# Kernel optimization log

Measured on AMD Instinct MI355X. Metric: run time of the kernel, lower is better.

The kernel has to match this reference:

```python
import jax, jax.numpy as jnp
import numpy as np

# irreps_in = irreps_out = 64x0e + 32x1o
MUL0, MUL1 = 64, 32          # multiplicities of 0e scalars and 1o vectors
DIM_IN = MUL0 + MUL1 * 3     # 160
N_NODES = 50000
IU0, IV0 = np.triu_indices(MUL0, k=1)   # 2016 scalar u<v pairs
IU1, IV1 = np.triu_indices(MUL1, k=1)   # 496 vector u<v pairs
# e3nn path normalization (component / element):
#   i_out=0 (0e): num_elements sum = 2016 + 64 + 496 + 32 = 2608, dim(0e)=1
#   i_out=1 (1o): num_elements = 32*64 = 2048, dim(1o)=3
C0 = float(np.sqrt(1.0 / 2608.0))
C1 = float(np.sqrt(3.0 / 2048.0))
INV_SQRT3 = float(1.0 / np.sqrt(3.0))   # w3j(1,0,1) and w3j(1,1,0) CG factor


def setup_inputs() -> dict:
    key = jax.random.key(0)
    ks = jax.random.split(key, 7)
    node_feats = jax.random.normal(ks[0], (N_NODES, DIM_IN), jnp.float32)
    node_messages = jax.random.normal(ks[1], (N_NODES, DIM_IN), jnp.float32)
    W1 = jax.random.normal(ks[2], (len(IU0), MUL0), jnp.float32)  # (0e,0e)->0e u<vw
    W2 = jax.random.normal(ks[3], (MUL0, MUL0), jnp.float32)      # (0e,0e)->0e uuw
    W3 = jax.random.normal(ks[4], (MUL1, MUL0, MUL1), jnp.float32)  # (1o,0e)->1o uvw
    W4 = jax.random.normal(ks[5], (len(IU1), MUL0), jnp.float32)  # (1o,1o)->0e u<vw
    W5 = jax.random.normal(ks[6], (MUL1, MUL0), jnp.float32)      # (1o,1o)->0e uuw
    return {"node_feats": node_feats, "node_messages": node_messages,
            "W1": W1, "W2": W2, "W3": W3, "W4": W4, "W5": W5}


def _tensor_square(x, W1, W2, W3, W4, W5):
    x0 = x[:, :MUL0]                        # [N, 64] scalars (0e)
    x1 = x[:, MUL0:].reshape(-1, MUL1, 3)   # [N, 32, 3] vectors (1o)
    # (0e x 0e) -> 0e
    pair0 = x0[:, IU0] * x0[:, IV0]         # [N, 2016]
    sq0 = x0 * x0                           # [N, 64]
    # (1o x 1o) -> 0e via dot products (w3j(1,1,0) = delta/sqrt3)
    d = jnp.einsum('nui,nvi->nuv', x1, x1)  # [N, 32, 32]
    pair1 = d[:, IU1, IV1] * INV_SQRT3      # [N, 496]
    diag1 = jnp.einsum('nui,nui->nu', x1, x1) * INV_SQRT3  # [N, 32]
    out0 = C0 * (pair0 @ W1 + sq0 @ W2 + pair1 @ W4 + diag1 @ W5)  # [N, 64]
    # (1o x 0e) -> 1o fully connected uvw (w3j(1,0,1) = eye/sqrt3)
    out1 = (C1 * INV_SQRT3) * jnp.einsum('nui,nv,uvw->nwi', x1, x0, W3)  # [N,32,3]
    return jnp.concatenate([out0, out1.reshape(-1, MUL1 * 3)], axis=1)


def reference(node_feats, node_messages, W1, W2, W3, W4, W5):
    x = node_feats + node_messages
    return _tensor_square(x, W1, W2, W3, W4, W5)
```

## Files before the change

kernel.cpp:

```cpp
#include <hip/hip_runtime.h>

typedef unsigned short u16;
typedef unsigned int u32;

#define N_NODES 50000
#define NB      64

#define BG_OFF  0
#define BT_OFF  262144
#define BH_OFF  327680

#define ASTR   72
#define AHSTR  40
#define XTSTR  68

typedef __attribute__((ext_vector_type(8))) short short8;
typedef __attribute__((ext_vector_type(4))) float f32x4;
union U4S8 { uint4 u; short8 s; };

__device__ __forceinline__ u16 f2bf(float f) {
    u32 u = __float_as_uint(f);
    return (u16)((u + 0x7fffu + ((u >> 16) & 1u)) >> 16);
}
__device__ __forceinline__ f32x4 bf4(uint2 q) {
    f32x4 r;
    r[0] = __uint_as_float(q.x << 16);
    r[1] = __uint_as_float(q.x & 0xffff0000u);
    r[2] = __uint_as_float(q.y << 16);
    r[3] = __uint_as_float(q.y & 0xffff0000u);
    return r;
}

__global__ __launch_bounds__(256)
void pack_kernel(const float* __restrict__ W1, const float* __restrict__ W2,
                 const float* __restrict__ W3, const float* __restrict__ W4,
                 const float* __restrict__ W5, u16* __restrict__ ws) {
    const float INV_SQRT3 = 0.57735026918962576f;
    int T = blockIdx.x * 256 + threadIdx.x;
    int slot0 = T * 8;
    float vals[8];
    if (slot0 < BT_OFF) {
        int ntile = slot0 >> 10, rem = slot0 & 1023;
        int ks = rem >> 9, q = (rem & 511) >> 3;
        int vbase = ks * 32 + (q >> 4) * 8;
        int j = ntile * 16 + (q & 15);
        int u = j >> 6, w = j & 63;
        #pragma unroll
        for (int jj = 0; jj < 8; ++jj) {
            int v = vbase + jj;
            if (v == u) vals[jj] = W2[u * 64 + w];
            else {
                int a = min(u, v), b = max(u, v);
                int p = a * (127 - a) / 2 + (b - a - 1);
                vals[jj] = 0.5f * W1[p * 64 + w];
            }
        }
    } else if (slot0 < BH_OFF) {
        int s = slot0 - BT_OFF;
        int ntile = s >> 10, rem = s & 1023;
        int ks = rem >> 9, q = (rem & 511) >> 3;
        int vbase = ks * 32 + (q >> 4) * 8;
        int j = ntile * 16 + (q & 15);
        int u = j >> 5, w = j & 31;
        #pragma unroll
        for (int jj = 0; jj < 8; ++jj)
            vals[jj] = W3[(u * 64 + (vbase + jj)) * 32 + w];
    } else {
        int s = slot0 - BH_OFF;
        int ntile = s >> 9, q = (s & 511) >> 3;
        int vbase = (q >> 4) * 8;
        int j = ntile * 16 + (q & 15);
        int u = j >> 6, w = j & 63;
        #pragma unroll
        for (int jj = 0; jj < 8; ++jj) {
            int v = vbase + jj;
            if (v == u) vals[jj] = W5[u * 64 + w] * INV_SQRT3;
            else {
                int a = min(u, v), b = max(u, v);
                int p = a * (63 - a) / 2 + (b - a - 1);
                vals[jj] = (0.5f * INV_SQRT3) * W4[p * 64 + w];
            }
        }
    }
    uint4 o;
    o.x = ((u32)f2bf(vals[1]) << 16) | f2bf(vals[0]);
    o.y = ((u32)f2bf(vals[3]) << 16) | f2bf(vals[2]);
    o.z = ((u32)f2bf(vals[5]) << 16) | f2bf(vals[4]);
    o.w = ((u32)f2bf(vals[7]) << 16) | f2bf(vals[6]);
    *(uint4*)(ws + slot0) = o;
}

__global__ __launch_bounds__(256, 3)
void node_block_kernel(const float* __restrict__ feats, const float* __restrict__ msgs,
                       const u16* __restrict__ ws, float* __restrict__ out) {
    __shared__ u16 A_S[64 * ASTR];
    __shared__ u16 A_H[192 * AHSTR];
    __shared__ u16 x0T[64 * XTSTR];
    __shared__ u16 x1T[96 * XTSTR];

    const int tid = threadIdx.x;
    const int node0 = blockIdx.x * NB;

    for (int k = 0; k < 5; ++k) {
        int chunk = tid + k * 256;
        int idx = chunk * 8;
        int n = (u32)idx / 160u;
        int d = idx - n * 160;
        int g = node0 * 160 + idx;
        float v[8];
        if (g + 8 <= N_NODES * 160) {
            float4 fa0 = *(const float4*)(feats + g);
            float4 fa1 = *(const float4*)(feats + g + 4);
            float4 fb0 = *(const float4*)(msgs + g);
            float4 fb1 = *(const float4*)(msgs + g + 4);
            v[0]=fa0.x+fb0.x; v[1]=fa0.y+fb0.y; v[2]=fa0.z+fb0.z; v[3]=fa0.w+fb0.w;
            v[4]=fa1.x+fb1.x; v[5]=fa1.y+fb1.y; v[6]=fa1.z+fb1.z; v[7]=fa1.w+fb1.w;
        } else {
            #pragma unroll
            for (int j = 0; j < 8; ++j) v[j] = 0.f;
        }
        u16 bv[8];
        #pragma unroll
        for (int j = 0; j < 8; ++j) bv[j] = f2bf(v[j]);
        if (d < 64) {
            uint4 pk;
            pk.x = ((u32)bv[1] << 16) | bv[0];
            pk.y = ((u32)bv[3] << 16) | bv[2];
            pk.z = ((u32)bv[5] << 16) | bv[4];
            pk.w = ((u32)bv[7] << 16) | bv[6];
            *(uint4*)&A_S[n * ASTR + d] = pk;
            #pragma unroll
            for (int j = 0; j < 8; ++j) x0T[(d + j) * XTSTR + n] = bv[j];
        } else {
            #pragma unroll
            for (int j = 0; j < 8; ++j) {
                int dd = d + j - 64;
                int u = (u32)dd / 3u, i = dd - u * 3;
                A_H[(i * 64 + n) * AHSTR + u] = bv[j];
                x1T[(u * 3 + i) * XTSTR + n] = bv[j];
            }
        }
    }
    __syncthreads();

    const int wave = tid >> 6, lane = tid & 63, quad = lane >> 4, l15 = lane & 15;
    const int wq = wave;
    const f32x4 z4 = {0.f, 0.f, 0.f, 0.f};
    const int ph64 = (blockIdx.x * 5) & 63;
    const int ph32 = (blockIdx.x * 5) & 31;

    f32x4 o0[4];
    #pragma unroll
    for (int mt = 0; mt < 4; ++mt) o0[mt] = z4;

    {
        short8 aS[4][2];
        #pragma unroll
        for (int mt = 0; mt < 4; ++mt)
            #pragma unroll
            for (int ks = 0; ks < 2; ++ks) {
                U4S8 t; t.u = *(const uint4*)&A_S[(mt * 16 + l15) * ASTR + ks * 32 + quad * 8];
                aS[mt][ks] = t.s;
            }
        const u16* bp = ws + BG_OFF + (u32)wq * 1024 + lane * 8;
        U4S8 b0[2], b1[2];
        b0[0].u = *(const uint4*)(bp + ph64 * 4096);
        b1[0].u = *(const uint4*)(bp + ph64 * 4096 + 512);
        {
            int p1 = ((ph64 + 1) & 63) * 4096;
            b0[1].u = *(const uint4*)(bp + p1);
            b1[1].u = *(const uint4*)(bp + p1 + 512);
        }
        #pragma unroll 2
        for (int t = 0; t < 64; ++t) {
            const int c = t & 1;
            const int u = (ph64 + t) & 63;
            short8 B0 = b0[c].s, B1 = b1[c].s;
            if (t < 62) {
                int pp = ((ph64 + t + 2) & 63) * 4096;
                b0[c].u = *(const uint4*)(bp + pp);
                b1[c].u = *(const uint4*)(bp + pp + 512);
            }
            f32x4 acc[4];
            #pragma unroll
            for (int mt = 0; mt < 4; ++mt) acc[mt] = z4;
            #pragma unroll
            for (int mt = 0; mt < 4; ++mt)
                acc[mt] = __builtin_amdgcn_mfma_f32_16x16x32_bf16(aS[mt][0], B0, acc[mt], 0, 0, 0);
            #pragma unroll
            for (int mt = 0; mt < 4; ++mt)
                acc[mt] = __builtin_amdgcn_mfma_f32_16x16x32_bf16(aS[mt][1], B1, acc[mt], 0, 0, 0);
            #pragma unroll
            for (int mt = 0; mt < 4; ++mt) {
                f32x4 xq = bf4(*(const uint2*)&x0T[u * XTSTR + mt * 16 + quad * 4]);
                o0[mt] += xq * acc[mt];
            }
        }
    }

    {
        short8 aH[12];
        #pragma unroll
        for (int m = 0; m < 12; ++m) {
            U4S8 t; t.u = *(const uint4*)&A_H[(m * 16 + l15) * AHSTR + quad * 8];
            aH[m] = t.s;
        }
        const u16* bp = ws + BH_OFF + (u32)wq * 512 + lane * 8;
        U4S8 bb[2];
        bb[0].u = *(const uint4*)(bp + ph32 * 2048);
        bb[1].u = *(const uint4*)(bp + ((ph32 + 1) & 31) * 2048);
        #pragma unroll 2
        for (int t = 0; t < 32; ++t) {
            const int c = t & 1;
            const int u = (ph32 + t) & 31;
            short8 B = bb[c].s;
            if (t < 30) bb[c].u = *(const uint4*)(bp + ((ph32 + t + 2) & 31) * 2048);
            #pragma unroll
            for (int i = 0; i < 3; ++i) {
                f32x4 acc[4];
                #pragma unroll
                for (int m = 0; m < 4; ++m) acc[m] = z4;
                #pragma unroll
                for (int m = 0; m < 4; ++m)
                    acc[m] = __builtin_amdgcn_mfma_f32_16x16x32_bf16(aH[i * 4 + m], B, acc[m], 0, 0, 0);
                #pragma unroll
                for (int m = 0; m < 4; ++m) {
                    f32x4 xq = bf4(*(const uint2*)&x1T[(u * 3 + i) * XTSTR + m * 16 + quad * 4]);
                    o0[m] += xq * acc[m];
                }
            }
        }
    }

    {
        const float C0v = 0.019581512f;
        #pragma unroll
        for (int mt = 0; mt < 4; ++mt)
            #pragma unroll
            for (int rr = 0; rr < 4; ++rr) {
                int node = node0 + mt * 16 + quad * 4 + rr;
                if (node < N_NODES)
                    out[node * 160 + wq * 16 + l15] = C0v * o0[mt][rr];
            }
    }

    {
        const int mh = wave >> 1, wh = wave & 1;
        short8 aT[2][2];
        #pragma unroll
        for (int m = 0; m < 2; ++m)
            #pragma unroll
            for (int ks = 0; ks < 2; ++ks) {
                U4S8 t; t.u = *(const uint4*)&A_S[((mh * 2 + m) * 16 + l15) * ASTR + ks * 32 + quad * 8];
                aT[m][ks] = t.s;
            }
        f32x4 o1[3][2];
        #pragma unroll
        for (int i = 0; i < 3; ++i)
            #pragma unroll
            for (int m = 0; m < 2; ++m) o1[i][m] = z4;

        const u16* bp = ws + BT_OFF + (u32)wh * 1024 + lane * 8;
        U4S8 b0[2], b1[2];
        b0[0].u = *(const uint4*)(bp + ph32 * 2048);
        b1[0].u = *(const uint4*)(bp + ph32 * 2048 + 512);
        {
            int p1 = ((ph32 + 1) & 31) * 2048;
            b0[1].u = *(const uint4*)(bp + p1);
            b1[1].u = *(const uint4*)(bp + p1 + 512);
        }
        #pragma unroll 2
        for (int t = 0; t < 32; ++t) {
            const int c = t & 1;
            const int u = (ph32 + t) & 31;
            short8 B0 = b0[c].s, B1 = b1[c].s;
            if (t < 30) {
                int pp = ((ph32 + t + 2) & 31) * 2048;
                b0[c].u = *(const uint4*)(bp + pp);
                b1[c].u = *(const uint4*)(bp + pp + 512);
            }
            f32x4 acc[2];
            #pragma unroll
            for (int m = 0; m < 2; ++m) acc[m] = z4;
            #pragma unroll
            for (int m = 0; m < 2; ++m)
                acc[m] = __builtin_amdgcn_mfma_f32_16x16x32_bf16(aT[m][0], B0, acc[m], 0, 0, 0);
            #pragma unroll
            for (int m = 0; m < 2; ++m)
                acc[m] = __builtin_amdgcn_mfma_f32_16x16x32_bf16(aT[m][1], B1, acc[m], 0, 0, 0);
            #pragma unroll
            for (int i = 0; i < 3; ++i)
                #pragma unroll
                for (int m = 0; m < 2; ++m) {
                    f32x4 xq = bf4(*(const uint2*)&x1T[(u * 3 + i) * XTSTR + (mh * 2 + m) * 16 + quad * 4]);
                    o1[i][m] += xq * acc[m];
                }
        }
        const float S1 = 0.022097087f;
        #pragma unroll
        for (int i = 0; i < 3; ++i)
            #pragma unroll
            for (int m = 0; m < 2; ++m)
                #pragma unroll
                for (int rr = 0; rr < 4; ++rr) {
                    int node = node0 + (mh * 2 + m) * 16 + quad * 4 + rr;
                    if (node < N_NODES)
                        out[node * 160 + 64 + (wh * 16 + l15) * 3 + i] = S1 * o1[i][m][rr];
                }
    }
}

extern "C" void kernel_launch(void* const* d_in, const int* in_sizes, int n_in,
                              void* d_out, int out_size, void* d_ws, size_t ws_size,
                              hipStream_t stream) {
    const float* feats = (const float*)d_in[0];
    const float* msgs  = (const float*)d_in[1];
    const float* W1    = (const float*)d_in[2];
    const float* W2    = (const float*)d_in[3];
    const float* W3    = (const float*)d_in[4];
    const float* W4    = (const float*)d_in[5];
    const float* W5    = (const float*)d_in[6];
    float* out = (float*)d_out;
    u16* ws = (u16*)d_ws;

    hipLaunchKernelGGL(pack_kernel, dim3(192), dim3(256), 0, stream,
                       W1, W2, W3, W4, W5, ws);
    hipLaunchKernelGGL(node_block_kernel, dim3((N_NODES + NB - 1) / NB), dim3(256), 0, stream,
                       feats, msgs, ws, out);
}
```

Measured before the change: 195.8 us.

## Regroup scalar/vector LDS tiles by node quads and process two u per iteration

Replaces the transposed x0T/x1T and A_H shared-memory layouts with node-quad grouped x0G/x1G arrays, so each lane fetches the x-values for two consecutive u with one 16-byte LDS read. The loops now handle two u per iteration with a deeper B-fragment prefetch. The A_H buffer is removed and its fragments are gathered element-wise from x1G. The smaller LDS footprint allows launch bounds to rise to 4 blocks per CU. The costs are more register pressure, slower scalar gathers for the aH fragments, and a different phase-stagger pattern across blocks.

```diff
diff --git a/kernel.cpp b/kernel.cpp
--- a/kernel.cpp
+++ b/kernel.cpp
@@ -11,8 +11,8 @@
 #define BH_OFF  327680
 
 #define ASTR   72
-#define AHSTR  40
-#define XTSTR  68
+#define X0STR  66
+#define X1STR  98
 
 typedef __attribute__((ext_vector_type(8))) short short8;
 typedef __attribute__((ext_vector_type(4))) float f32x4;
@@ -90,13 +90,12 @@
     *(uint4*)(ws + slot0) = o;
 }
 
-__global__ __launch_bounds__(256, 3)
+__global__ __launch_bounds__(256, 4)
 void node_block_kernel(const float* __restrict__ feats, const float* __restrict__ msgs,
                        const u16* __restrict__ ws, float* __restrict__ out) {
     __shared__ u16 A_S[64 * ASTR];
-    __shared__ u16 A_H[192 * AHSTR];
-    __shared__ u16 x0T[64 * XTSTR];
-    __shared__ u16 x1T[96 * XTSTR];
+    __shared__ u16 x0G[16 * X0STR * 4];
+    __shared__ u16 x1G[16 * X1STR * 4];
 
     const int tid = threadIdx.x;
     const int node0 = blockIdx.x * NB;
@@ -129,15 +128,15 @@
             pk.z = ((u32)bv[5] << 16) | bv[4];
             pk.w = ((u32)bv[7] << 16) | bv[6];
             *(uint4*)&A_S[n * ASTR + d] = pk;
-            #pragma unroll
-            for (int j = 0; j < 8; ++j) x0T[(d + j) * XTSTR + n] = bv[j];
+            int b0 = ((n >> 2) * X0STR + d) * 4 + (n & 3);
+            #pragma unroll
+            for (int j = 0; j < 8; ++j) x0G[b0 + j * 4] = bv[j];
         } else {
             #pragma unroll
             for (int j = 0; j < 8; ++j) {
                 int dd = d + j - 64;
                 int u = (u32)dd / 3u, i = dd - u * 3;
-                A_H[(i * 64 + n) * AHSTR + u] = bv[j];
-                x1T[(u * 3 + i) * XTSTR + n] = bv[j];
+                x1G[((n >> 2) * X1STR + i * 32 + u) * 4 + (n & 3)] = bv[j];
             }
         }
     }
@@ -146,8 +145,8 @@
     const int wave = tid >> 6, lane = tid & 63, quad = lane >> 4, l15 = lane & 15;
     const int wq = wave;
     const f32x4 z4 = {0.f, 0.f, 0.f, 0.f};
-    const int ph64 = (blockIdx.x * 5) & 63;
-    const int ph32 = (blockIdx.x * 5) & 31;
+    const int ph64 = (blockIdx.x * 10) & 62;
+    const int ph32 = ph64 & 30;
 
     f32x4 o0[4];
     #pragma unroll
@@ -163,37 +162,52 @@
                 aS[mt][ks] = t.s;
             }
         const u16* bp = ws + BG_OFF + (u32)wq * 1024 + lane * 8;
-        U4S8 b0[2], b1[2];
-        b0[0].u = *(const uint4*)(bp + ph64 * 4096);
-        b1[0].u = *(const uint4*)(bp + ph64 * 4096 + 512);
-        {
-            int p1 = ((ph64 + 1) & 63) * 4096;
-            b0[1].u = *(const uint4*)(bp + p1);
-            b1[1].u = *(const uint4*)(bp + p1 + 512);
-        }
+        U4S8 bS[2][2][2];
+        #pragma unroll
+        for (int buf = 0; buf < 2; ++buf)
+            #pragma unroll
+            for (int tp = 0; tp < 2; ++tp) {
+                int u = (ph64 + buf * 2 + tp) & 63;
+                bS[buf][tp][0].u = *(const uint4*)(bp + u * 4096);
+                bS[buf][tp][1].u = *(const uint4*)(bp + u * 4096 + 512);
+            }
         #pragma unroll 2
-        for (int t = 0; t < 64; ++t) {
-            const int c = t & 1;
-            const int u = (ph64 + t) & 63;
-            short8 B0 = b0[c].s, B1 = b1[c].s;
-            if (t < 62) {
-                int pp = ((ph64 + t + 2) & 63) * 4096;
-                b0[c].u = *(const uint4*)(bp + pp);
-                b1[c].u = *(const uint4*)(bp + pp + 512);
+        for (int p = 0; p < 32; ++p) {
+            const int c = p & 1;
+            const int u0 = (ph64 + 2 * p) & 63;
+            uint4 xg[4];
+            #pragma unroll
+            for (int mt = 0; mt < 4; ++mt)
+                xg[mt] = *(const uint4*)&x0G[((mt * 4 + quad) * X0STR + u0) * 4];
+            short8 B00 = bS[c][0][0].s, B01 = bS[c][0][1].s;
+            short8 B10 = bS[c][1][0].s, B11 = bS[c][1][1].s;
+            if (p < 30) {
+                int ua = (ph64 + 2 * p + 4) & 63;
+                bS[c][0][0].u = *(const uint4*)(bp + ua * 4096);
+                bS[c][0][1].u = *(const uint4*)(bp + ua * 4096 + 512);
+                bS[c][1][0].u = *(const uint4*)(bp + (ua + 1) * 4096);
+                bS[c][1][1].u = *(const uint4*)(bp + (ua + 1) * 4096 + 512);
             }
             f32x4 acc[4];
             #pragma unroll
-            for (int mt = 0; mt < 4; ++mt) acc[mt] = z4;
-            #pragma unroll
-            for (int mt = 0; mt < 4; ++mt)
-                acc[mt] = __builtin_amdgcn_mfma_f32_16x16x32_bf16(aS[mt][0], B0, acc[mt], 0, 0, 0);
-            #pragma unroll
-            for (int mt = 0; mt < 4; ++mt)
-                acc[mt] = __builtin_amdgcn_mfma_f32_16x16x32_bf16(aS[mt][1], B1, acc[mt], 0, 0, 0);
-            #pragma unroll
             for (int mt = 0; mt < 4; ++mt) {
-                f32x4 xq = bf4(*(const uint2*)&x0T[u * XTSTR + mt * 16 + quad * 4]);
-                o0[mt] += xq * acc[mt];
+                acc[mt] = __builtin_amdgcn_mfma_f32_16x16x32_bf16(aS[mt][0], B00, z4, 0, 0, 0);
+                acc[mt] = __builtin_amdgcn_mfma_f32_16x16x32_bf16(aS[mt][1], B01, acc[mt], 0, 0, 0);
+            }
+            #pragma unroll
+            for (int mt = 0; mt < 4; ++mt) {
+                uint2 q; q.x = xg[mt].x; q.y = xg[mt].y;
+                o0[mt] += bf4(q) * acc[mt];
+            }
+            #pragma unroll
+            for (int mt = 0; mt < 4; ++mt) {
+                acc[mt] = __builtin_amdgcn_mfma_f32_16x16x32_bf16(aS[mt][0], B10, z4, 0, 0, 0);
+                acc[mt] = __builtin_amdgcn_mfma_f32_16x16x32_bf16(aS[mt][1], B11, acc[mt], 0, 0, 0);
+            }
+            #pragma unroll
+            for (int mt = 0; mt < 4; ++mt) {
+                uint2 q; q.x = xg[mt].z; q.y = xg[mt].w;
+                o0[mt] += bf4(q) * acc[mt];
             }
         }
     }
@@ -201,32 +215,56 @@
     {
         short8 aH[12];
         #pragma unroll
-        for (int m = 0; m < 12; ++m) {
-            U4S8 t; t.u = *(const uint4*)&A_H[(m * 16 + l15) * AHSTR + quad * 8];
-            aH[m] = t.s;
-        }
+        for (int i = 0; i < 3; ++i)
+            #pragma unroll
+            for (int m = 0; m < 4; ++m) {
+                const int n = m * 16 + l15;
+                const int base = ((n >> 2) * X1STR + i * 32) * 4 + (n & 3);
+                union { short8 s; u16 e[8]; } t;
+                #pragma unroll
+                for (int j = 0; j < 8; ++j)
+                    t.e[j] = x1G[base + (quad * 8 + j) * 4];
+                aH[i * 4 + m] = t.s;
+            }
         const u16* bp = ws + BH_OFF + (u32)wq * 512 + lane * 8;
-        U4S8 bb[2];
-        bb[0].u = *(const uint4*)(bp + ph32 * 2048);
-        bb[1].u = *(const uint4*)(bp + ((ph32 + 1) & 31) * 2048);
+        U4S8 bH[2][2];
+        #pragma unroll
+        for (int buf = 0; buf < 2; ++buf)
+            #pragma unroll
+            for (int tp = 0; tp < 2; ++tp)
+                bH[buf][tp].u = *(const uint4*)(bp + ((ph32 + buf * 2 + tp) & 31) * 2048);
         #pragma unroll 2
-        for (int t = 0; t < 32; ++t) {
-            const int c = t & 1;
-            const int u = (ph32 + t) & 31;
-            short8 B = bb[c].s;
-            if (t < 30) bb[c].u = *(const uint4*)(bp + ((ph32 + t + 2) & 31) * 2048);
+        for (int p = 0; p < 16; ++p) {
+            const int c = p & 1;
+            const int u0 = (ph32 + 2 * p) & 31;
+            short8 B0 = bH[c][0].s, B1 = bH[c][1].s;
+            if (p < 14) {
+                int ua = (ph32 + 2 * p + 4) & 31;
+                bH[c][0].u = *(const uint4*)(bp + ua * 2048);
+                bH[c][1].u = *(const uint4*)(bp + (ua + 1) * 2048);
+            }
             #pragma unroll
             for (int i = 0; i < 3; ++i) {
+                uint4 xg[4];
+                #pragma unroll
+                for (int m = 0; m < 4; ++m)
+                    xg[m] = *(const uint4*)&x1G[((m * 4 + quad) * X1STR + i * 32 + u0) * 4];
                 f32x4 acc[4];
                 #pragma unroll
-                for (int m = 0; m < 4; ++m) acc[m] = z4;
-                #pragma unroll
                 for (int m = 0; m < 4; ++m)
-                    acc[m] = __builtin_amdgcn_mfma_f32_16x16x32_bf16(aH[i * 4 + m], B, acc[m], 0, 0, 0);
+                    acc[m] = __builtin_amdgcn_mfma_f32_16x16x32_bf16(aH[i * 4 + m], B0, z4, 0, 0, 0);
                 #pragma unroll
                 for (int m = 0; m < 4; ++m) {
-                    f32x4 xq = bf4(*(const uint2*)&x1T[(u * 3 + i) * XTSTR + m * 16 + quad * 4]);
-                    o0[m] += xq * acc[m];
+                    uint2 q; q.x = xg[m].x; q.y = xg[m].y;
+                    o0[m] += bf4(q) * acc[m];
+                }
+                #pragma unroll
+                for (int m = 0; m < 4; ++m)
+                    acc[m] = __builtin_amdgcn_mfma_f32_16x16x32_bf16(aH[i * 4 + m], B1, z4, 0, 0, 0);
+                #pragma unroll
+                for (int m = 0; m < 4; ++m) {
+                    uint2 q; q.x = xg[m].z; q.y = xg[m].w;
+                    o0[m] += bf4(q) * acc[m];
                 }
             }
         }
@@ -261,39 +299,58 @@
             for (int m = 0; m < 2; ++m) o1[i][m] = z4;
 
         const u16* bp = ws + BT_OFF + (u32)wh * 1024 + lane * 8;
-        U4S8 b0[2], b1[2];
-        b0[0].u = *(const uint4*)(bp + ph32 * 2048);
-        b1[0].u = *(const uint4*)(bp + ph32 * 2048 + 512);
-        {
-            int p1 = ((ph32 + 1) & 31) * 2048;
-            b0[1].u = *(const uint4*)(bp + p1);
-            b1[1].u = *(const uint4*)(bp + p1 + 512);
-        }
+        U4S8 bT[2][2][2];
+        #pragma unroll
+        for (int buf = 0; buf < 2; ++buf)
+            #pragma unroll
+            for (int tp = 0; tp < 2; ++tp) {
+                int u = (ph32 + buf * 2 + tp) & 31;
+                bT[buf][tp][0].u = *(const uint4*)(bp + u * 2048);
+                bT[buf][tp][1].u = *(const uint4*)(bp + u * 2048 + 512);
+            }
         #pragma unroll 2
-        for (int t = 0; t < 32; ++t) {
-            const int c = t & 1;
-            const int u = (ph32 + t) & 31;
-            short8 B0 = b0[c].s, B1 = b1[c].s;
-            if (t < 30) {
-                int pp = ((ph32 + t + 2) & 31) * 2048;
-                b0[c].u = *(const uint4*)(bp + pp);
-                b1[c].u = *(const uint4*)(bp + pp + 512);
+        for (int p = 0; p < 16; ++p) {
+            const int c = p & 1;
+            const int u0 = (ph32 + 2 * p) & 31;
+            uint4 xg[3][2];
+            #pragma unroll
+            for (int i = 0; i < 3; ++i)
+                #pragma unroll
+                for (int m = 0; m < 2; ++m)
+                    xg[i][m] = *(const uint4*)&x1G[(((mh * 2 + m) * 4 + quad) * X1STR + i * 32 + u0) * 4];
+            short8 B00 = bT[c][0][0].s, B01 = bT[c][0][1].s;
+            short8 B10 = bT[c][1][0].s, B11 = bT[c][1][1].s;
+            if (p < 14) {
+                int ua = (ph32 + 2 * p + 4) & 31;
+                bT[c][0][0].u = *(const uint4*)(bp + ua * 2048);
+                bT[c][0][1].u = *(const uint4*)(bp + ua * 2048 + 512);
+                bT[c][1][0].u = *(const uint4*)(bp + (ua + 1) * 2048);
+                bT[c][1][1].u = *(const uint4*)(bp + (ua + 1) * 2048 + 512);
             }
             f32x4 acc[2];
             #pragma unroll
-            for (int m = 0; m < 2; ++m) acc[m] = z4;
-            #pragma unroll
-            for (int m = 0; m < 2; ++m)
-                acc[m] = __builtin_amdgcn_mfma_f32_16x16x32_bf16(aT[m][0], B0, acc[m], 0, 0, 0);
-            #pragma unroll
-            for (int m = 0; m < 2; ++m)
-                acc[m] = __builtin_amdgcn_mfma_f32_16x16x32_bf16(aT[m][1], B1, acc[m], 0, 0, 0);
+            for (int m = 0; m < 2; ++m) {
+                acc[m] = __builtin_amdgcn_mfma_f32_16x16x32_bf16(aT[m][0], B00, z4, 0, 0, 0);
+                acc[m] = __builtin_amdgcn_mfma_f32_16x16x32_bf16(aT[m][1], B01, acc[m], 0, 0, 0);
+            }
             #pragma unroll
             for (int i = 0; i < 3; ++i)
                 #pragma unroll
                 for (int m = 0; m < 2; ++m) {
-                    f32x4 xq = bf4(*(const uint2*)&x1T[(u * 3 + i) * XTSTR + (mh * 2 + m) * 16 + quad * 4]);
-                    o1[i][m] += xq * acc[m];
+                    uint2 q; q.x = xg[i][m].x; q.y = xg[i][m].y;
+                    o1[i][m] += bf4(q) * acc[m];
+                }
+            #pragma unroll
+            for (int m = 0; m < 2; ++m) {
+                acc[m] = __builtin_amdgcn_mfma_f32_16x16x32_bf16(aT[m][0], B10, z4, 0, 0, 0);
+                acc[m] = __builtin_amdgcn_mfma_f32_16x16x32_bf16(aT[m][1], B11, acc[m], 0, 0, 0);
+            }
+            #pragma unroll
+            for (int i = 0; i < 3; ++i)
+                #pragma unroll
+                for (int m = 0; m < 2; ++m) {
+                    uint2 q; q.x = xg[i][m].z; q.y = xg[i][m].w;
+                    o1[i][m] += bf4(q) * acc[m];
                 }
         }
         const float S1 = 0.022097087f;
```

Result: slower. 623.3 us (+218.3%).
